# Kernel tuning notes

Measured on AMD Instinct MI355X. Metric: run time of the kernel, lower is better.

## Reference

```python
import jax, jax.numpy as jnp
import numpy as np

H = 128
N_NODES = 100000
N_EDGES = 400000
N_INC = 800000
BN_EPS = 1e-5


def _bn_relu(x, g, b):
    # BatchNorm1d in training mode: batch mean + biased variance, then affine + ReLU
    m = x.mean(0)
    v = x.var(0)
    return jax.nn.relu(g * (x - m) * jax.lax.rsqrt(v + BN_EPS) + b)


def setup_inputs() -> dict:
    key = jax.random.key(0)
    ks = jax.random.split(key, 12)
    s1 = 1.0 / np.sqrt(2 * H)
    s2 = 1.0 / np.sqrt(H)
    inp = {
        "node_rep": jax.random.normal(ks[0], (N_NODES, H), jnp.float32),
        "edge_rep": jax.random.normal(ks[1], (N_EDGES, H), jnp.float32),
        "node_idx": jax.random.randint(ks[2], (N_INC,), 0, N_NODES),
        "edge_idx": jax.random.randint(ks[3], (N_INC,), 0, N_EDGES),
        # lvl_mlp_1: Linear(2H->H, no bias) + BN + ReLU
        "W1": jax.random.uniform(ks[4], (2 * H, H), jnp.float32, -s1, s1),
        "g1": jnp.ones((H,), jnp.float32), "b1": jnp.zeros((H,), jnp.float32),
        # lvl_mlp_2: two (Linear(H->H,no bias)+BN+ReLU) blocks
        "W2a": jax.random.uniform(ks[5], (H, H), jnp.float32, -s2, s2),
        "g2a": jnp.ones((H,), jnp.float32), "b2a": jnp.zeros((H,), jnp.float32),
        "W2b": jax.random.uniform(ks[6], (H, H), jnp.float32, -s2, s2),
        "g2b": jnp.ones((H,), jnp.float32), "b2b": jnp.zeros((H,), jnp.float32),
        # lift_mlp: two (Linear(H->H,no bias)+BN+ReLU) blocks
        "W3a": jax.random.uniform(ks[7], (H, H), jnp.float32, -s2, s2),
        "g3a": jnp.ones((H,), jnp.float32), "b3a": jnp.zeros((H,), jnp.float32),
        "W3b": jax.random.uniform(ks[8], (H, H), jnp.float32, -s2, s2),
        "g3b": jnp.ones((H,), jnp.float32), "b3b": jnp.zeros((H,), jnp.float32),
        "eps1": jnp.zeros((), jnp.float32),
        "eps2": jnp.zeros((), jnp.float32),
    }
    return inp


def reference(node_rep, edge_rep, node_idx, edge_idx,
              W1, g1, b1, W2a, g2a, b2a, W2b, g2b, b2b,
              W3a, g3a, b3a, W3b, g3b, b3b, eps1, eps2):
    n2e_val = node_rep[node_idx]                          # [M,H] gather
    msg = jnp.concatenate([n2e_val, edge_rep[edge_idx]], -1)  # [M,2H]
    msg = _bn_relu(msg @ W1, g1, b1)                      # lvl_mlp_1 -> [M,H]
    cat = jax.ops.segment_sum(jnp.concatenate([msg, n2e_val], -1),
                              edge_idx, num_segments=edge_rep.shape[0])  # [E,2H]
    lvl_aggr_edge = cat[:, :H][edge_idx] - msg            # [M,H]
    lift_aggr = cat[:, H:]                                # [E,H]
    lvl_aggr = jax.ops.segment_sum(lvl_aggr_edge, node_idx,
                                   num_segments=node_rep.shape[0])  # [N,H]
    x = (1.0 + eps1) * node_rep + lvl_aggr
    node_out = _bn_relu(_bn_relu(x @ W2a, g2a, b2a) @ W2b, g2b, b2b)
    y = (1.0 + eps2) * edge_rep + lift_aggr
    edge_out = _bn_relu(_bn_relu(y @ W3a, g3a, b3a) @ W3b, g3b, b3b)
    return node_out, edge_out
```

## Files before the change

kernel.cpp:

```cpp
#include <hip/hip_runtime.h>

#define H 128
#define N_NODES 100000
#define N_EDGES 400000
#define N_INC   800000
#define BN_EPS 1e-5f

typedef __attribute__((ext_vector_type(8))) __bf16 bf16x8;
typedef __attribute__((ext_vector_type(4))) float f32x4;

__device__ __forceinline__ float4 ld4(const float* p) { return *(const float4*)p; }
__device__ __forceinline__ void st4(float* p, float4 v) { *(float4*)p = v; }
__device__ __forceinline__ float4 bnrelu4(float4 p, float4 sc, float4 sf) {
    float4 o;
    o.x = fmaxf(fmaf(p.x, sc.x, sf.x), 0.f);
    o.y = fmaxf(fmaf(p.y, sc.y, sf.y), 0.f);
    o.z = fmaxf(fmaf(p.z, sc.z, sf.z), 0.f);
    o.w = fmaxf(fmaf(p.w, sc.w, sf.w), 0.f);
    return o;
}
__device__ __forceinline__ unsigned short f2bf(float x) {
    unsigned int u = __builtin_bit_cast(unsigned int, x);
    u += 0x7fffu + ((u >> 16) & 1u);
    return (unsigned short)(u >> 16);
}
__device__ __forceinline__ float bf2f(unsigned short s) {
    unsigned int u = ((unsigned int)s) << 16;
    return __builtin_bit_cast(float, u);
}

__device__ __forceinline__ void split8(const float* a, bf16x8& h, bf16x8& l) {
#pragma unroll
    for (int j = 0; j < 8; ++j) h[j] = (__bf16)a[j];
#pragma unroll
    for (int j = 0; j < 8; ++j) l[j] = (__bf16)(a[j] - (float)h[j]);
}

__global__ void wtrans_kernel(const float* __restrict__ W, unsigned short* __restrict__ Wt,
                              int kbits)
{
    int i = blockIdx.x * 256 + threadIdx.x;
    int K = 1 << kbits;
    int n = i >> kbits;
    int k = i & (K - 1);
    Wt[i] = f2bf(W[(size_t)k * H + n]);
}


__global__ __launch_bounds__(256) void gemm1_mfma(
    const float* __restrict__ node_rep, const float* __restrict__ edge_rep,
    const int* __restrict__ node_idx, const int* __restrict__ edge_idx,
    const unsigned short* __restrict__ Wt,
    unsigned short* __restrict__ out, float* __restrict__ sums)
{
    const int tid = threadIdx.x;
    const int lane = tid & 63;
    const int wv = tid >> 6;
    const int l15 = lane & 15;
    const int kb = lane >> 4;
    const int ko = kb * 8;
    const int rowBase = blockIdx.x * 128 + wv * 32;
    const int r0 = rowBase + l15;
    const int r1 = rowBase + 16 + l15;
    const float* an0 = node_rep + (size_t)node_idx[r0] * H;
    const float* ae0 = edge_rep + (size_t)edge_idx[r0] * H;
    const float* an1 = node_rep + (size_t)node_idx[r1] * H;
    const float* ae1 = edge_rep + (size_t)edge_idx[r1] * H;

    f32x4 acc[2][8];
#pragma unroll
    for (int i = 0; i < 2; ++i)
#pragma unroll
        for (int j = 0; j < 8; ++j) acc[i][j] = (f32x4){0.f, 0.f, 0.f, 0.f};

#pragma unroll
    for (int ks = 0; ks < 8; ++ks) {
        const int k0 = ks * 32 + ko;
        const float* p0 = (ks < 4) ? (an0 + k0) : (ae0 + (k0 - 128));
        const float* p1 = (ks < 4) ? (an1 + k0) : (ae1 + (k0 - 128));
        float a0[8], a1[8];
        { float4 x = ld4(p0), y = ld4(p0 + 4);
          a0[0]=x.x; a0[1]=x.y; a0[2]=x.z; a0[3]=x.w; a0[4]=y.x; a0[5]=y.y; a0[6]=y.z; a0[7]=y.w; }
        { float4 x = ld4(p1), y = ld4(p1 + 4);
          a1[0]=x.x; a1[1]=x.y; a1[2]=x.z; a1[3]=x.w; a1[4]=y.x; a1[5]=y.y; a1[6]=y.z; a1[7]=y.w; }
        bf16x8 h0, l0, h1, l1;
        split8(a0, h0, l0);
        split8(a1, h1, l1);
        const unsigned short* wp = Wt + (size_t)l15 * 256 + ks * 32 + ko;
#pragma unroll
        for (int ct = 0; ct < 8; ++ct) {
            bf16x8 bw = *(const bf16x8*)(wp + ct * 16 * 256);
            acc[0][ct] = __builtin_amdgcn_mfma_f32_16x16x32_bf16(h0, bw, acc[0][ct], 0, 0, 0);
            acc[0][ct] = __builtin_amdgcn_mfma_f32_16x16x32_bf16(l0, bw, acc[0][ct], 0, 0, 0);
            acc[1][ct] = __builtin_amdgcn_mfma_f32_16x16x32_bf16(h1, bw, acc[1][ct], 0, 0, 0);
            acc[1][ct] = __builtin_amdgcn_mfma_f32_16x16x32_bf16(l1, bw, acc[1][ct], 0, 0, 0);
        }
    }

    __shared__ float sred[4][256];
    float scol[8], qcol[8];
#pragma unroll
    for (int ct = 0; ct < 8; ++ct) { scol[ct] = 0.f; qcol[ct] = 0.f; }
#pragma unroll
    for (int rt = 0; rt < 2; ++rt) {
        const int rg = rowBase + rt * 16 + kb * 4;
#pragma unroll
        for (int j = 0; j < 4; ++j) {
#pragma unroll
            for (int ct = 0; ct < 8; ++ct) {
                unsigned short us = f2bf(acc[rt][ct][j]);
                out[(size_t)(rg + j) * H + ct * 16 + l15] = us;
                float v = bf2f(us);
                scol[ct] += v;
                qcol[ct] = fmaf(v, v, qcol[ct]);
            }
        }
    }
#pragma unroll
    for (int ct = 0; ct < 8; ++ct) {
        scol[ct] += __shfl_xor(scol[ct], 16);
        scol[ct] += __shfl_xor(scol[ct], 32);
        qcol[ct] += __shfl_xor(qcol[ct], 16);
        qcol[ct] += __shfl_xor(qcol[ct], 32);
    }
    if (kb == 0) {
#pragma unroll
        for (int ct = 0; ct < 8; ++ct) {
            sred[wv][ct * 16 + l15] = scol[ct];
            sred[wv][128 + ct * 16 + l15] = qcol[ct];
        }
    }
    __syncthreads();
    float tot = sred[0][tid & 255] + sred[1][tid & 255] + sred[2][tid & 255] + sred[3][tid & 255];
    atomicAdd(&sums[tid & 255], tot);
}

__global__ __launch_bounds__(256) void gemmh_mfma(
    int M, int mode, const float* __restrict__ A0, const float* __restrict__ ss,
    const unsigned short* __restrict__ Wt,
    float* __restrict__ out, float* __restrict__ sums)
{
    const int tid = threadIdx.x;
    const int lane = tid & 63;
    const int wv = tid >> 6;
    const int l15 = lane & 15;
    const int kb = lane >> 4;
    const int ko = kb * 8;
    const int rowBase = blockIdx.x * 128 + wv * 32;
    int r0 = rowBase + l15;       if (r0 >= M) r0 = M - 1;
    int r1 = rowBase + 16 + l15;  if (r1 >= M) r1 = M - 1;
    const float* a0p = A0 + (size_t)r0 * H;
    const float* a1p = A0 + (size_t)r1 * H;

    f32x4 acc[2][8];
#pragma unroll
    for (int i = 0; i < 2; ++i)
#pragma unroll
        for (int j = 0; j < 8; ++j) acc[i][j] = (f32x4){0.f, 0.f, 0.f, 0.f};

#pragma unroll
    for (int ks = 0; ks < 4; ++ks) {
        const int k0 = ks * 32 + ko;
        float a0[8], a1[8];
        { float4 x = ld4(a0p + k0), y = ld4(a0p + k0 + 4);
          a0[0]=x.x; a0[1]=x.y; a0[2]=x.z; a0[3]=x.w; a0[4]=y.x; a0[5]=y.y; a0[6]=y.z; a0[7]=y.w; }
        { float4 x = ld4(a1p + k0), y = ld4(a1p + k0 + 4);
          a1[0]=x.x; a1[1]=x.y; a1[2]=x.z; a1[3]=x.w; a1[4]=y.x; a1[5]=y.y; a1[6]=y.z; a1[7]=y.w; }
        if (mode == 2) {
            float4 sca = ld4(&ss[k0]), scb = ld4(&ss[k0 + 4]);
            float4 sfa = ld4(&ss[128 + k0]), sfb = ld4(&ss[128 + k0 + 4]);
            float sc[8] = {sca.x, sca.y, sca.z, sca.w, scb.x, scb.y, scb.z, scb.w};
            float sf[8] = {sfa.x, sfa.y, sfa.z, sfa.w, sfb.x, sfb.y, sfb.z, sfb.w};
#pragma unroll
            for (int j = 0; j < 8; ++j) {
                a0[j] = fmaxf(fmaf(a0[j], sc[j], sf[j]), 0.f);
                a1[j] = fmaxf(fmaf(a1[j], sc[j], sf[j]), 0.f);
            }
        }
        bf16x8 h0, l0, h1, l1;
        split8(a0, h0, l0);
        split8(a1, h1, l1);
        const unsigned short* wp = Wt + (size_t)l15 * 128 + ks * 32 + ko;
#pragma unroll
        for (int ct = 0; ct < 8; ++ct) {
            bf16x8 bw = *(const bf16x8*)(wp + ct * 16 * 128);
            acc[0][ct] = __builtin_amdgcn_mfma_f32_16x16x32_bf16(h0, bw, acc[0][ct], 0, 0, 0);
            acc[0][ct] = __builtin_amdgcn_mfma_f32_16x16x32_bf16(l0, bw, acc[0][ct], 0, 0, 0);
            acc[1][ct] = __builtin_amdgcn_mfma_f32_16x16x32_bf16(h1, bw, acc[1][ct], 0, 0, 0);
            acc[1][ct] = __builtin_amdgcn_mfma_f32_16x16x32_bf16(l1, bw, acc[1][ct], 0, 0, 0);
        }
    }

    __shared__ float sred[4][256];
    float scol[8], qcol[8];
#pragma unroll
    for (int ct = 0; ct < 8; ++ct) { scol[ct] = 0.f; qcol[ct] = 0.f; }
#pragma unroll
    for (int rt = 0; rt < 2; ++rt) {
#pragma unroll
        for (int j = 0; j < 4; ++j) {
            const int rg = rowBase + rt * 16 + kb * 4 + j;
            if (rg < M) {
#pragma unroll
                for (int ct = 0; ct < 8; ++ct) {
                    float v = acc[rt][ct][j];
                    out[(size_t)rg * H + ct * 16 + l15] = v;
                    scol[ct] += v;
                    qcol[ct] = fmaf(v, v, qcol[ct]);
                }
            }
        }
    }
#pragma unroll
    for (int ct = 0; ct < 8; ++ct) {
        scol[ct] += __shfl_xor(scol[ct], 16);
        scol[ct] += __shfl_xor(scol[ct], 32);
        qcol[ct] += __shfl_xor(qcol[ct], 16);
        qcol[ct] += __shfl_xor(qcol[ct], 32);
    }
    if (kb == 0) {
#pragma unroll
        for (int ct = 0; ct < 8; ++ct) {
            sred[wv][ct * 16 + l15] = scol[ct];
            sred[wv][128 + ct * 16 + l15] = qcol[ct];
        }
    }
    __syncthreads();
    float tot = sred[0][tid & 255] + sred[1][tid & 255] + sred[2][tid & 255] + sred[3][tid & 255];
    atomicAdd(&sums[tid & 255], tot);
}

__global__ void finalize_kernel(const float* __restrict__ sums, float invM,
                                const float* __restrict__ g, const float* __restrict__ b,
                                float* __restrict__ ss)
{
    int c = threadIdx.x;
    float mean = sums[c] * invM;
    float var = fmaf(-mean, mean, sums[128 + c] * invM);
    float scale = g[c] * rsqrtf(var + BN_EPS);
    ss[c] = scale;
    ss[128 + c] = fmaf(-mean, scale, b[c]);
}

__global__ void hist_kernel(const int* __restrict__ idx, int* __restrict__ cnt, int n)
{
    int i = blockIdx.x * 256 + threadIdx.x;
    if (i < n) atomicAdd(&cnt[idx[i]], 1);
}

__global__ __launch_bounds__(256) void scan_block_kernel(int* __restrict__ a, int n,
                                                         int* __restrict__ aux)
{
    __shared__ int sh[2048];
    __shared__ int ts[256];
    const int t = threadIdx.x;
    const int base = blockIdx.x * 2048;
#pragma unroll
    for (int k = 0; k < 8; ++k) {
        int i = base + t + k * 256;
        sh[t + k * 256] = (i < n) ? a[i] : 0;
    }
    __syncthreads();
    int loc[8], sum = 0;
#pragma unroll
    for (int k = 0; k < 8; ++k) { loc[k] = sh[t * 8 + k]; sum += loc[k]; }
    ts[t] = sum;
    __syncthreads();
    for (int o = 1; o < 256; o <<= 1) {
        int v = (t >= o) ? ts[t - o] : 0;
        __syncthreads();
        ts[t] += v;
        __syncthreads();
    }
    int run = ts[t] - sum;
#pragma unroll
    for (int k = 0; k < 8; ++k) {
        int i = base + t * 8 + k;
        if (i < n) a[i] = run;
        run += loc[k];
    }
    if (aux != nullptr && t == 255) aux[blockIdx.x] = ts[255];
}

__global__ void scan_add_kernel(int* __restrict__ a, int n, const int* __restrict__ aux)
{
    int i = blockIdx.x * 256 + threadIdx.x;
    if (i < n) a[i] += aux[i >> 11];
}

__global__ void fill_kernel(const int* __restrict__ idx, int* __restrict__ off,
                            int* __restrict__ list, int n)
{
    int i = blockIdx.x * 256 + threadIdx.x;
    if (i < n) {
        int p = atomicAdd(&off[idx[i]], 1);
        list[p] = i;
    }
}

__global__ __launch_bounds__(256) void gather_edge_kernel(
    const unsigned short* __restrict__ msg, const float* __restrict__ node_rep,
    const float* __restrict__ edge_rep, const int* __restrict__ node_idx,
    const int* __restrict__ eoff, const int* __restrict__ elist,
    const float* __restrict__ ss, const float* __restrict__ eps2p,
    float* __restrict__ catm, float* __restrict__ yedge)
{
    const int t = threadIdx.x;
    const int sub = t >> 5;
    const int lane = t & 31;
    const int e = blockIdx.x * 8 + sub;
    const int c = lane * 4;
    const int s = (e == 0) ? 0 : eoff[e - 1];
    const int en = eoff[e];
    const float4 sc = ld4(&ss[c]);
    const float4 sf = ld4(&ss[128 + c]);
    float4 macc = make_float4(0.f, 0.f, 0.f, 0.f);
    float4 lacc = make_float4(0.f, 0.f, 0.f, 0.f);
    int idx = (s < en) ? elist[s] : 0;
    for (int j = s; j < en; ++j) {
        int idxn = (j + 1 < en) ? elist[j + 1] : 0;
        int n = node_idx[idx];
        ushort4 mb = *(const ushort4*)(msg + (size_t)idx * H + c);
        float4 nv = ld4(&node_rep[(size_t)n * H + c]);
        float4 p = make_float4(bf2f(mb.x), bf2f(mb.y), bf2f(mb.z), bf2f(mb.w));
        float4 m = bnrelu4(p, sc, sf);
        macc.x += m.x; macc.y += m.y; macc.z += m.z; macc.w += m.w;
        lacc.x += nv.x; lacc.y += nv.y; lacc.z += nv.z; lacc.w += nv.w;
        idx = idxn;
    }
    st4(&catm[(size_t)e * H + c], macc);
    const float eps = eps2p[0];
    float4 er = ld4(&edge_rep[(size_t)e * H + c]);
    float4 y;
    y.x = fmaf(eps, er.x, er.x + lacc.x);
    y.y = fmaf(eps, er.y, er.y + lacc.y);
    y.z = fmaf(eps, er.z, er.z + lacc.z);
    y.w = fmaf(eps, er.w, er.w + lacc.w);
    st4(&yedge[(size_t)e * H + c], y);
}

__global__ __launch_bounds__(256) void gather_node_kernel(
    const unsigned short* __restrict__ msg, const float* __restrict__ catm,
    const float* __restrict__ node_rep, const int* __restrict__ edge_idx,
    const int* __restrict__ noff, const int* __restrict__ nlist,
    const float* __restrict__ ss, const float* __restrict__ eps1p,
    float* __restrict__ xnode)
{
    const int t = threadIdx.x;
    const int sub = t >> 5;
    const int lane = t & 31;
    const int n = blockIdx.x * 8 + sub;
    const int c = lane * 4;
    const int s = (n == 0) ? 0 : noff[n - 1];
    const int en = noff[n];
    const float4 sc = ld4(&ss[c]);
    const float4 sf = ld4(&ss[128 + c]);
    float4 acc = make_float4(0.f, 0.f, 0.f, 0.f);
    int idx = (s < en) ? nlist[s] : 0;
    for (int j = s; j < en; ++j) {
        int idxn = (j + 1 < en) ? nlist[j + 1] : 0;
        int e = edge_idx[idx];
        ushort4 mb = *(const ushort4*)(msg + (size_t)idx * H + c);
        float4 cv = ld4(&catm[(size_t)e * H + c]);
        float4 p = make_float4(bf2f(mb.x), bf2f(mb.y), bf2f(mb.z), bf2f(mb.w));
        float4 m = bnrelu4(p, sc, sf);
        acc.x += cv.x - m.x; acc.y += cv.y - m.y;
        acc.z += cv.z - m.z; acc.w += cv.w - m.w;
        idx = idxn;
    }
    const float eps = eps1p[0];
    float4 nr = ld4(&node_rep[(size_t)n * H + c]);
    float4 x;
    x.x = fmaf(eps, nr.x, nr.x + acc.x);
    x.y = fmaf(eps, nr.y, nr.y + acc.y);
    x.z = fmaf(eps, nr.z, nr.z + acc.z);
    x.w = fmaf(eps, nr.w, nr.w + acc.w);
    st4(&xnode[(size_t)n * H + c], x);
}

__global__ __launch_bounds__(256) void apply_kernel(const float* __restrict__ pre,
                                                    const float* __restrict__ ss,
                                                    float* __restrict__ out, int M)
{
    size_t gid = (size_t)blockIdx.x * 256 + threadIdx.x;
    size_t r = gid >> 5;
    int c = (int)(gid & 31) * 4;
    if (r >= (size_t)M) return;
    float4 p = ld4(&pre[r * H + c]);
    float4 sc = ld4(&ss[c]);
    float4 sf = ld4(&ss[128 + c]);
    st4(&out[r * H + c], bnrelu4(p, sc, sf));
}

extern "C" void kernel_launch(void* const* d_in, const int* in_sizes, int n_in,
                              void* d_out, int out_size, void* d_ws, size_t ws_size,
                              hipStream_t stream)
{
    const float* node_rep = (const float*)d_in[0];
    const float* edge_rep = (const float*)d_in[1];
    const int*   node_idx = (const int*)d_in[2];
    const int*   edge_idx = (const int*)d_in[3];
    const float* W1  = (const float*)d_in[4];
    const float* g1  = (const float*)d_in[5];
    const float* b1  = (const float*)d_in[6];
    const float* W2a = (const float*)d_in[7];
    const float* g2a = (const float*)d_in[8];
    const float* b2a = (const float*)d_in[9];
    const float* W2b = (const float*)d_in[10];
    const float* g2b = (const float*)d_in[11];
    const float* b2b = (const float*)d_in[12];
    const float* W3a = (const float*)d_in[13];
    const float* g3a = (const float*)d_in[14];
    const float* b3a = (const float*)d_in[15];
    const float* W3b = (const float*)d_in[16];
    const float* g3b = (const float*)d_in[17];
    const float* b3b = (const float*)d_in[18];
    const float* eps1 = (const float*)d_in[19];
    const float* eps2 = (const float*)d_in[20];

    float* ws = (float*)d_ws;
    unsigned short* msgb = (unsigned short*)ws;
    float* catm  = ws + (size_t) 51200000;
    float* yedge = ws + (size_t)102400000;
    float* xnode = ws + (size_t)153600000;
    int* eoff  = (int*)(ws + (size_t)153600000);
    int* elist = (int*)(ws + (size_t)154000000);
    float* stat = ws + (size_t)166400000;
    int* noff  = (int*)(ws + (size_t)166402560);
    int* nlist = (int*)(ws + (size_t)166502560);
    int* eaux  = (int*)(ws + (size_t)167302560);
    int* naux  = (int*)(ws + (size_t)167302816);
    unsigned short* wt1  = (unsigned short*)(ws + (size_t)167304000);
    unsigned short* wt2a = (unsigned short*)(ws + (size_t)167320384);
    unsigned short* wt2b = (unsigned short*)(ws + (size_t)167328576);
    unsigned short* wt3a = (unsigned short*)(ws + (size_t)167336768);
    unsigned short* wt3b = (unsigned short*)(ws + (size_t)167344960);

    float* e1 = catm;
    float* e2 = (float*)msgb;
    float* n1 = catm;
    float* n2 = catm + (size_t)12800000;

    float* sums0 = stat +    0; float* ss0 = stat + 1280;
    float* sums1 = stat +  256; float* ss1 = stat + 1536;
    float* sums2 = stat +  512; float* ss2 = stat + 1792;
    float* sums3 = stat +  768; float* ss3 = stat + 2048;
    float* sums4 = stat + 1024; float* ss4 = stat + 2304;

    float* out_node = (float*)d_out;
    float* out_edge = out_node + (size_t)N_NODES * H;

    hipMemsetAsync(stat, 0, 1280 * sizeof(float), stream);
    hipMemsetAsync(eoff, 0, (size_t)N_EDGES * sizeof(int), stream);
    hipMemsetAsync(noff, 0, (size_t)N_NODES * sizeof(int), stream);

    wtrans_kernel<<<128, 256, 0, stream>>>(W1,  wt1,  8);
    wtrans_kernel<<< 64, 256, 0, stream>>>(W2a, wt2a, 7);
    wtrans_kernel<<< 64, 256, 0, stream>>>(W2b, wt2b, 7);
    wtrans_kernel<<< 64, 256, 0, stream>>>(W3a, wt3a, 7);
    wtrans_kernel<<< 64, 256, 0, stream>>>(W3b, wt3b, 7);

    hist_kernel<<<N_INC / 256, 256, 0, stream>>>(edge_idx, eoff, N_INC);
    scan_block_kernel<<<196, 256, 0, stream>>>(eoff, N_EDGES, eaux);
    scan_block_kernel<<<1, 256, 0, stream>>>(eaux, 196, nullptr);
    scan_add_kernel<<<(N_EDGES + 255) / 256, 256, 0, stream>>>(eoff, N_EDGES, eaux);
    fill_kernel<<<N_INC / 256, 256, 0, stream>>>(edge_idx, eoff, elist, N_INC);

    hist_kernel<<<N_INC / 256, 256, 0, stream>>>(node_idx, noff, N_INC);
    scan_block_kernel<<<49, 256, 0, stream>>>(noff, N_NODES, naux);
    scan_block_kernel<<<1, 256, 0, stream>>>(naux, 49, nullptr);
    scan_add_kernel<<<(N_NODES + 255) / 256, 256, 0, stream>>>(noff, N_NODES, naux);
    fill_kernel<<<N_INC / 256, 256, 0, stream>>>(node_idx, noff, nlist, N_INC);

    gemm1_mfma<<<N_INC / 128, 256, 0, stream>>>(node_rep, edge_rep, node_idx, edge_idx,
                                                wt1, msgb, sums0);
    finalize_kernel<<<1, 128, 0, stream>>>(sums0, 1.0f / N_INC, g1, b1, ss0);

    gather_edge_kernel<<<N_EDGES / 8, 256, 0, stream>>>(msgb, node_rep, edge_rep, node_idx,
                                                        eoff, elist, ss0, eps2, catm, yedge);
    gather_node_kernel<<<N_NODES / 8, 256, 0, stream>>>(msgb, catm, node_rep, edge_idx,
                                                        noff, nlist, ss0, eps1, xnode);

    gemmh_mfma<<<N_EDGES / 128, 256, 0, stream>>>(N_EDGES, 0, yedge, nullptr, wt3a, e1, sums3);
    finalize_kernel<<<1, 128, 0, stream>>>(sums3, 1.0f / N_EDGES, g3a, b3a, ss3);
    gemmh_mfma<<<N_EDGES / 128, 256, 0, stream>>>(N_EDGES, 2, e1, ss3, wt3b, e2, sums4);
    finalize_kernel<<<1, 128, 0, stream>>>(sums4, 1.0f / N_EDGES, g3b, b3b, ss4);
    apply_kernel<<<N_EDGES / 8, 256, 0, stream>>>(e2, ss4, out_edge, N_EDGES);

    gemmh_mfma<<<(N_NODES + 127) / 128, 256, 0, stream>>>(N_NODES, 0, xnode, nullptr, wt2a, n1, sums1);
    finalize_kernel<<<1, 128, 0, stream>>>(sums1, 1.0f / N_NODES, g2a, b2a, ss1);
    gemmh_mfma<<<(N_NODES + 127) / 128, 256, 0, stream>>>(N_NODES, 2, n1, ss1, wt2b, n2, sums2);
    finalize_kernel<<<1, 128, 0, stream>>>(sums2, 1.0f / N_NODES, g2b, b2b, ss2);
    apply_kernel<<<N_NODES / 8, 256, 0, stream>>>(n2, ss2, out_node, N_NODES);
}
```

Baseline: 1.822 ms.

## Stage weights in swizzled LDS, use persistent blocks, and prefetch A tiles

Each GEMM kernel now copies its transposed bf16 weight matrix into LDS once per block, with an XOR swizzle against bank conflicts. The grid becomes persistent: a fixed number of blocks loop over row tiles and keep BN column statistics in registers, so there are fewer atomics and less weight reloading. A three-slot register buffer prefetches A rows two k-steps ahead to hide gather latency. The cost is a large LDS footprint (64KB for gemm1) that limits occupancy, plus more registers per thread.

Result: faster. 1.715 ms (-5.9%).

```diff
diff --git a/kernel.cpp b/kernel.cpp
--- a/kernel.cpp
+++ b/kernel.cpp
@@ -53,69 +53,94 @@
     const unsigned short* __restrict__ Wt,
     unsigned short* __restrict__ out, float* __restrict__ sums)
 {
+    __shared__ unsigned short Wl[128 * 256];
     const int tid = threadIdx.x;
     const int lane = tid & 63;
     const int wv = tid >> 6;
     const int l15 = lane & 15;
     const int kb = lane >> 4;
     const int ko = kb * 8;
-    const int rowBase = blockIdx.x * 128 + wv * 32;
-    const int r0 = rowBase + l15;
-    const int r1 = rowBase + 16 + l15;
-    const float* an0 = node_rep + (size_t)node_idx[r0] * H;
-    const float* ae0 = edge_rep + (size_t)edge_idx[r0] * H;
-    const float* an1 = node_rep + (size_t)node_idx[r1] * H;
-    const float* ae1 = edge_rep + (size_t)edge_idx[r1] * H;
-
-    f32x4 acc[2][8];
-#pragma unroll
-    for (int i = 0; i < 2; ++i)
-#pragma unroll
-        for (int j = 0; j < 8; ++j) acc[i][j] = (f32x4){0.f, 0.f, 0.f, 0.f};
-
-#pragma unroll
-    for (int ks = 0; ks < 8; ++ks) {
-        const int k0 = ks * 32 + ko;
-        const float* p0 = (ks < 4) ? (an0 + k0) : (ae0 + (k0 - 128));
-        const float* p1 = (ks < 4) ? (an1 + k0) : (ae1 + (k0 - 128));
-        float a0[8], a1[8];
-        { float4 x = ld4(p0), y = ld4(p0 + 4);
-          a0[0]=x.x; a0[1]=x.y; a0[2]=x.z; a0[3]=x.w; a0[4]=y.x; a0[5]=y.y; a0[6]=y.z; a0[7]=y.w; }
-        { float4 x = ld4(p1), y = ld4(p1 + 4);
-          a1[0]=x.x; a1[1]=x.y; a1[2]=x.z; a1[3]=x.w; a1[4]=y.x; a1[5]=y.y; a1[6]=y.z; a1[7]=y.w; }
-        bf16x8 h0, l0, h1, l1;
-        split8(a0, h0, l0);
-        split8(a1, h1, l1);
-        const unsigned short* wp = Wt + (size_t)l15 * 256 + ks * 32 + ko;
-#pragma unroll
-        for (int ct = 0; ct < 8; ++ct) {
-            bf16x8 bw = *(const bf16x8*)(wp + ct * 16 * 256);
-            acc[0][ct] = __builtin_amdgcn_mfma_f32_16x16x32_bf16(h0, bw, acc[0][ct], 0, 0, 0);
-            acc[0][ct] = __builtin_amdgcn_mfma_f32_16x16x32_bf16(l0, bw, acc[0][ct], 0, 0, 0);
-            acc[1][ct] = __builtin_amdgcn_mfma_f32_16x16x32_bf16(h1, bw, acc[1][ct], 0, 0, 0);
-            acc[1][ct] = __builtin_amdgcn_mfma_f32_16x16x32_bf16(l1, bw, acc[1][ct], 0, 0, 0);
+    const int swz = (l15 & 7) << 3;
+
+#pragma unroll
+    for (int it = 0; it < 16; ++it) {
+        int g = it * 256 + tid;
+        int n = g >> 5, k8 = (g & 31) * 8;
+        *(uint4*)&Wl[n * 256 + (k8 ^ ((n & 7) << 3))] = *(const uint4*)&Wt[(size_t)n * 256 + k8];
+    }
+    __syncthreads();
+
+    float scol[8], qcol[8];
+#pragma unroll
+    for (int ct = 0; ct < 8; ++ct) { scol[ct] = 0.f; qcol[ct] = 0.f; }
+
+    for (int rb = blockIdx.x; rb < N_INC / 128; rb += gridDim.x) {
+        const int rowBase = rb * 128 + wv * 32;
+        const int r0 = rowBase + l15;
+        const int r1 = rowBase + 16 + l15;
+        const float* an0 = node_rep + (size_t)node_idx[r0] * H + ko;
+        const float* ae0 = edge_rep + (size_t)edge_idx[r0] * H + ko;
+        const float* an1 = node_rep + (size_t)node_idx[r1] * H + ko;
+        const float* ae1 = edge_rep + (size_t)edge_idx[r1] * H + ko;
+
+        f32x4 acc[2][8];
+#pragma unroll
+        for (int i = 0; i < 2; ++i)
+#pragma unroll
+            for (int j = 0; j < 8; ++j) acc[i][j] = (f32x4){0.f, 0.f, 0.f, 0.f};
+
+        float4 ab[3][2][2];
+        ab[0][0][0] = ld4(an0);      ab[0][0][1] = ld4(an0 + 4);
+        ab[0][1][0] = ld4(an1);      ab[0][1][1] = ld4(an1 + 4);
+        ab[1][0][0] = ld4(an0 + 32); ab[1][0][1] = ld4(an0 + 36);
+        ab[1][1][0] = ld4(an1 + 32); ab[1][1][1] = ld4(an1 + 36);
+
+#pragma unroll
+        for (int ks = 0; ks < 8; ++ks) {
+            if (ks < 6) {
+                const int kf = (ks + 2) * 32;
+                const float* p0 = (ks + 2 < 4) ? an0 + kf : ae0 + (kf - 128);
+                const float* p1 = (ks + 2 < 4) ? an1 + kf : ae1 + (kf - 128);
+                const int slot = (ks + 2) % 3;
+                ab[slot][0][0] = ld4(p0); ab[slot][0][1] = ld4(p0 + 4);
+                ab[slot][1][0] = ld4(p1); ab[slot][1][1] = ld4(p1 + 4);
+            }
+            const int cur = ks % 3;
+            float a0[8] = {ab[cur][0][0].x, ab[cur][0][0].y, ab[cur][0][0].z, ab[cur][0][0].w,
+                           ab[cur][0][1].x, ab[cur][0][1].y, ab[cur][0][1].z, ab[cur][0][1].w};
+            float a1[8] = {ab[cur][1][0].x, ab[cur][1][0].y, ab[cur][1][0].z, ab[cur][1][0].w,
+                           ab[cur][1][1].x, ab[cur][1][1].y, ab[cur][1][1].z, ab[cur][1][1].w};
+            bf16x8 h0, l0, h1, l1;
+            split8(a0, h0, l0);
+            split8(a1, h1, l1);
+            const int kbase = (ks * 32 + ko) ^ swz;
+#pragma unroll
+            for (int ct = 0; ct < 8; ++ct) {
+                bf16x8 bw = *(const bf16x8*)&Wl[(ct * 16 + l15) * 256 + kbase];
+                acc[0][ct] = __builtin_amdgcn_mfma_f32_16x16x32_bf16(h0, bw, acc[0][ct], 0, 0, 0);
+                acc[0][ct] = __builtin_amdgcn_mfma_f32_16x16x32_bf16(l0, bw, acc[0][ct], 0, 0, 0);
+                acc[1][ct] = __builtin_amdgcn_mfma_f32_16x16x32_bf16(h1, bw, acc[1][ct], 0, 0, 0);
+                acc[1][ct] = __builtin_amdgcn_mfma_f32_16x16x32_bf16(l1, bw, acc[1][ct], 0, 0, 0);
+            }
         }
-    }
-
-    __shared__ float sred[4][256];
-    float scol[8], qcol[8];
-#pragma unroll
-    for (int ct = 0; ct < 8; ++ct) { scol[ct] = 0.f; qcol[ct] = 0.f; }
-#pragma unroll
-    for (int rt = 0; rt < 2; ++rt) {
-        const int rg = rowBase + rt * 16 + kb * 4;
-#pragma unroll
-        for (int j = 0; j < 4; ++j) {
-#pragma unroll
-            for (int ct = 0; ct < 8; ++ct) {
-                unsigned short us = f2bf(acc[rt][ct][j]);
-                out[(size_t)(rg + j) * H + ct * 16 + l15] = us;
-                float v = bf2f(us);
-                scol[ct] += v;
-                qcol[ct] = fmaf(v, v, qcol[ct]);
+
+#pragma unroll
+        for (int rt = 0; rt < 2; ++rt) {
+            const int rg0 = rowBase + rt * 16 + kb * 4;
+#pragma unroll
+            for (int j = 0; j < 4; ++j) {
+#pragma unroll
+                for (int ct = 0; ct < 8; ++ct) {
+                    unsigned short us = f2bf(acc[rt][ct][j]);
+                    out[(size_t)(rg0 + j) * H + ct * 16 + l15] = us;
+                    float v = bf2f(us);
+                    scol[ct] += v;
+                    qcol[ct] = fmaf(v, v, qcol[ct]);
+                }
             }
         }
     }
+
 #pragma unroll
     for (int ct = 0; ct < 8; ++ct) {
         scol[ct] += __shfl_xor(scol[ct], 16);
@@ -123,94 +148,123 @@
         qcol[ct] += __shfl_xor(qcol[ct], 16);
         qcol[ct] += __shfl_xor(qcol[ct], 32);
     }
+    __syncthreads();
+    float* sred = (float*)Wl;
     if (kb == 0) {
 #pragma unroll
         for (int ct = 0; ct < 8; ++ct) {
-            sred[wv][ct * 16 + l15] = scol[ct];
-            sred[wv][128 + ct * 16 + l15] = qcol[ct];
+            sred[wv * 256 + ct * 16 + l15] = scol[ct];
+            sred[wv * 256 + 128 + ct * 16 + l15] = qcol[ct];
         }
     }
     __syncthreads();
-    float tot = sred[0][tid & 255] + sred[1][tid & 255] + sred[2][tid & 255] + sred[3][tid & 255];
-    atomicAdd(&sums[tid & 255], tot);
-}
-
-__global__ __launch_bounds__(256) void gemmh_mfma(
+    float tot = sred[tid] + sred[256 + tid] + sred[512 + tid] + sred[768 + tid];
+    atomicAdd(&sums[tid], tot);
+}
+
+__global__ __launch_bounds__(256, 3) void gemmh_mfma(
     int M, int mode, const float* __restrict__ A0, const float* __restrict__ ss,
     const unsigned short* __restrict__ Wt,
     float* __restrict__ out, float* __restrict__ sums)
 {
+    __shared__ unsigned short Wl[128 * 128];
     const int tid = threadIdx.x;
     const int lane = tid & 63;
     const int wv = tid >> 6;
     const int l15 = lane & 15;
     const int kb = lane >> 4;
     const int ko = kb * 8;
-    const int rowBase = blockIdx.x * 128 + wv * 32;
-    int r0 = rowBase + l15;       if (r0 >= M) r0 = M - 1;
-    int r1 = rowBase + 16 + l15;  if (r1 >= M) r1 = M - 1;
-    const float* a0p = A0 + (size_t)r0 * H;
-    const float* a1p = A0 + (size_t)r1 * H;
-
-    f32x4 acc[2][8];
-#pragma unroll
-    for (int i = 0; i < 2; ++i)
-#pragma unroll
-        for (int j = 0; j < 8; ++j) acc[i][j] = (f32x4){0.f, 0.f, 0.f, 0.f};
-
-#pragma unroll
-    for (int ks = 0; ks < 4; ++ks) {
-        const int k0 = ks * 32 + ko;
-        float a0[8], a1[8];
-        { float4 x = ld4(a0p + k0), y = ld4(a0p + k0 + 4);
-          a0[0]=x.x; a0[1]=x.y; a0[2]=x.z; a0[3]=x.w; a0[4]=y.x; a0[5]=y.y; a0[6]=y.z; a0[7]=y.w; }
-        { float4 x = ld4(a1p + k0), y = ld4(a1p + k0 + 4);
-          a1[0]=x.x; a1[1]=x.y; a1[2]=x.z; a1[3]=x.w; a1[4]=y.x; a1[5]=y.y; a1[6]=y.z; a1[7]=y.w; }
-        if (mode == 2) {
-            float4 sca = ld4(&ss[k0]), scb = ld4(&ss[k0 + 4]);
-            float4 sfa = ld4(&ss[128 + k0]), sfb = ld4(&ss[128 + k0 + 4]);
-            float sc[8] = {sca.x, sca.y, sca.z, sca.w, scb.x, scb.y, scb.z, scb.w};
-            float sf[8] = {sfa.x, sfa.y, sfa.z, sfa.w, sfb.x, sfb.y, sfb.z, sfb.w};
-#pragma unroll
-            for (int j = 0; j < 8; ++j) {
-                a0[j] = fmaxf(fmaf(a0[j], sc[j], sf[j]), 0.f);
-                a1[j] = fmaxf(fmaf(a1[j], sc[j], sf[j]), 0.f);
+    const int swz = (l15 & 7) << 3;
+    const int nTiles = (M + 127) >> 7;
+
+#pragma unroll
+    for (int it = 0; it < 8; ++it) {
+        int g = it * 256 + tid;
+        int n = g >> 4, k8 = (g & 15) * 8;
+        *(uint4*)&Wl[n * 128 + (k8 ^ ((n & 7) << 3))] = *(const uint4*)&Wt[(size_t)n * 128 + k8];
+    }
+    __syncthreads();
+
+    float scol[8], qcol[8];
+#pragma unroll
+    for (int ct = 0; ct < 8; ++ct) { scol[ct] = 0.f; qcol[ct] = 0.f; }
+
+    for (int rb = blockIdx.x; rb < nTiles; rb += gridDim.x) {
+        const int rowBase = rb * 128 + wv * 32;
+        int r0 = rowBase + l15;       if (r0 >= M) r0 = M - 1;
+        int r1 = rowBase + 16 + l15;  if (r1 >= M) r1 = M - 1;
+        const float* a0p = A0 + (size_t)r0 * H + ko;
+        const float* a1p = A0 + (size_t)r1 * H + ko;
+
+        f32x4 acc[2][8];
+#pragma unroll
+        for (int i = 0; i < 2; ++i)
+#pragma unroll
+            for (int j = 0; j < 8; ++j) acc[i][j] = (f32x4){0.f, 0.f, 0.f, 0.f};
+
+        float4 ab[3][2][2];
+        ab[0][0][0] = ld4(a0p);      ab[0][0][1] = ld4(a0p + 4);
+        ab[0][1][0] = ld4(a1p);      ab[0][1][1] = ld4(a1p + 4);
+        ab[1][0][0] = ld4(a0p + 32); ab[1][0][1] = ld4(a0p + 36);
+        ab[1][1][0] = ld4(a1p + 32); ab[1][1][1] = ld4(a1p + 36);
+
+#pragma unroll
+        for (int ks = 0; ks < 4; ++ks) {
+            if (ks < 2) {
+                const int kf = (ks + 2) * 32;
+                const int slot = (ks + 2) % 3;
+                ab[slot][0][0] = ld4(a0p + kf); ab[slot][0][1] = ld4(a0p + kf + 4);
+                ab[slot][1][0] = ld4(a1p + kf); ab[slot][1][1] = ld4(a1p + kf + 4);
+            }
+            const int cur = ks % 3;
+            float a0[8] = {ab[cur][0][0].x, ab[cur][0][0].y, ab[cur][0][0].z, ab[cur][0][0].w,
+                           ab[cur][0][1].x, ab[cur][0][1].y, ab[cur][0][1].z, ab[cur][0][1].w};
+            float a1[8] = {ab[cur][1][0].x, ab[cur][1][0].y, ab[cur][1][0].z, ab[cur][1][0].w,
+                           ab[cur][1][1].x, ab[cur][1][1].y, ab[cur][1][1].z, ab[cur][1][1].w};
+            if (mode == 2) {
+                const int k0 = ks * 32 + ko;
+                float4 sca = ld4(&ss[k0]), scb = ld4(&ss[k0 + 4]);
+                float4 sfa = ld4(&ss[128 + k0]), sfb = ld4(&ss[128 + k0 + 4]);
+                float sc[8] = {sca.x, sca.y, sca.z, sca.w, scb.x, scb.y, scb.z, scb.w};
+                float sf[8] = {sfa.x, sfa.y, sfa.z, sfa.w, sfb.x, sfb.y, sfb.z, sfb.w};
+#pragma unroll
+                for (int j = 0; j < 8; ++j) {
+                    a0[j] = fmaxf(fmaf(a0[j], sc[j], sf[j]), 0.f);
+                    a1[j] = fmaxf(fmaf(a1[j], sc[j], sf[j]), 0.f);
+                }
+            }
+            bf16x8 h0, l0, h1, l1;
+            split8(a0, h0, l0);
+            split8(a1, h1, l1);
+            const int kbase = (ks * 32 + ko) ^ swz;
+#pragma unroll
+            for (int ct = 0; ct < 8; ++ct) {
+                bf16x8 bw = *(const bf16x8*)&Wl[(ct * 16 + l15) * 128 + kbase];
+                acc[0][ct] = __builtin_amdgcn_mfma_f32_16x16x32_bf16(h0, bw, acc[0][ct], 0, 0, 0);
+                acc[0][ct] = __builtin_amdgcn_mfma_f32_16x16x32_bf16(l0, bw, acc[0][ct], 0, 0, 0);
+                acc[1][ct] = __builtin_amdgcn_mfma_f32_16x16x32_bf16(h1, bw, acc[1][ct], 0, 0, 0);
+                acc[1][ct] = __builtin_amdgcn_mfma_f32_16x16x32_bf16(l1, bw, acc[1][ct], 0, 0, 0);
             }
         }
-        bf16x8 h0, l0, h1, l1;
-        split8(a0, h0, l0);
-        split8(a1, h1, l1);
-        const unsigned short* wp = Wt + (size_t)l15 * 128 + ks * 32 + ko;
-#pragma unroll
-        for (int ct = 0; ct < 8; ++ct) {
-            bf16x8 bw = *(const bf16x8*)(wp + ct * 16 * 128);
-            acc[0][ct] = __builtin_amdgcn_mfma_f32_16x16x32_bf16(h0, bw, acc[0][ct], 0, 0, 0);
-            acc[0][ct] = __builtin_amdgcn_mfma_f32_16x16x32_bf16(l0, bw, acc[0][ct], 0, 0, 0);
-            acc[1][ct] = __builtin_amdgcn_mfma_f32_16x16x32_bf16(h1, bw, acc[1][ct], 0, 0, 0);
-            acc[1][ct] = __builtin_amdgcn_mfma_f32_16x16x32_bf16(l1, bw, acc[1][ct], 0, 0, 0);
+
+#pragma unroll
+        for (int rt = 0; rt < 2; ++rt) {
+#pragma unroll
+            for (int j = 0; j < 4; ++j) {
+                const int rg = rowBase + rt * 16 + kb * 4 + j;
+                if (rg < M) {
+#pragma unroll
+                    for (int ct = 0; ct < 8; ++ct) {
+                        float v = acc[rt][ct][j];
+                        out[(size_t)rg * H + ct * 16 + l15] = v;
+                        scol[ct] += v;
+                        qcol[ct] = fmaf(v, v, qcol[ct]);
+                    }
+                }
+            }
         }
     }
 
-    __shared__ float sred[4][256];
-    float scol[8], qcol[8];
-#pragma unroll
-    for (int ct = 0; ct < 8; ++ct) { scol[ct] = 0.f; qcol[ct] = 0.f; }
-#pragma unroll
-    for (int rt = 0; rt < 2; ++rt) {
-#pragma unroll
-        for (int j = 0; j < 4; ++j) {
-            const int rg = rowBase + rt * 16 + kb * 4 + j;
-            if (rg < M) {
-#pragma unroll
-                for (int ct = 0; ct < 8; ++ct) {
-                    float v = acc[rt][ct][j];
-                    out[(size_t)rg * H + ct * 16 + l15] = v;
-                    scol[ct] += v;
-                    qcol[ct] = fmaf(v, v, qcol[ct]);
-                }
-            }
-        }
-    }
 #pragma unroll
     for (int ct = 0; ct < 8; ++ct) {
         scol[ct] += __shfl_xor(scol[ct], 16);
@@ -218,16 +272,18 @@
         qcol[ct] += __shfl_xor(qcol[ct], 16);
         qcol[ct] += __shfl_xor(qcol[ct], 32);
     }
+    __syncthreads();
+    float* sred = (float*)Wl;
     if (kb == 0) {
 #pragma unroll
         for (int ct = 0; ct < 8; ++ct) {
-            sred[wv][ct * 16 + l15] = scol[ct];
-            sred[wv][128 + ct * 16 + l15] = qcol[ct];
+            sred[wv * 256 + ct * 16 + l15] = scol[ct];
+            sred[wv * 256 + 128 + ct * 16 + l15] = qcol[ct];
         }
     }
     __syncthreads();
-    float tot = sred[0][tid & 255] + sred[1][tid & 255] + sred[2][tid & 255] + sred[3][tid & 255];
-    atomicAdd(&sums[tid & 255], tot);
+    float tot = sred[tid] + sred[256 + tid] + sred[512 + tid] + sred[768 + tid];
+    atomicAdd(&sums[tid], tot);
 }
 
 __global__ void finalize_kernel(const float* __restrict__ sums, float invM,
@@ -472,8 +528,8 @@
     scan_add_kernel<<<(N_NODES + 255) / 256, 256, 0, stream>>>(noff, N_NODES, naux);
     fill_kernel<<<N_INC / 256, 256, 0, stream>>>(node_idx, noff, nlist, N_INC);
 
-    gemm1_mfma<<<N_INC / 128, 256, 0, stream>>>(node_rep, edge_rep, node_idx, edge_idx,
-                                                wt1, msgb, sums0);
+    gemm1_mfma<<<512, 256, 0, stream>>>(node_rep, edge_rep, node_idx, edge_idx,
+                                        wt1, msgb, sums0);
     finalize_kernel<<<1, 128, 0, stream>>>(sums0, 1.0f / N_INC, g1, b1, ss0);
 
     gather_edge_kernel<<<N_EDGES / 8, 256, 0, stream>>>(msgb, node_rep, edge_rep, node_idx,
@@ -481,15 +537,15 @@
     gather_node_kernel<<<N_NODES / 8, 256, 0, stream>>>(msgb, catm, node_rep, edge_idx,
                                                         noff, nlist, ss0, eps1, xnode);
 
-    gemmh_mfma<<<N_EDGES / 128, 256, 0, stream>>>(N_EDGES, 0, yedge, nullptr, wt3a, e1, sums3);
+    gemmh_mfma<<<768, 256, 0, stream>>>(N_EDGES, 0, yedge, nullptr, wt3a, e1, sums3);
     finalize_kernel<<<1, 128, 0, stream>>>(sums3, 1.0f / N_EDGES, g3a, b3a, ss3);
-    gemmh_mfma<<<N_EDGES / 128, 256, 0, stream>>>(N_EDGES, 2, e1, ss3, wt3b, e2, sums4);
+    gemmh_mfma<<<768, 256, 0, stream>>>(N_EDGES, 2, e1, ss3, wt3b, e2, sums4);
     finalize_kernel<<<1, 128, 0, stream>>>(sums4, 1.0f / N_EDGES, g3b, b3b, ss4);
     apply_kernel<<<N_EDGES / 8, 256, 0, stream>>>(e2, ss4, out_edge, N_EDGES);
 
-    gemmh_mfma<<<(N_NODES + 127) / 128, 256, 0, stream>>>(N_NODES, 0, xnode, nullptr, wt2a, n1, sums1);
+    gemmh_mfma<<<768, 256, 0, stream>>>(N_NODES, 0, xnode, nullptr, wt2a, n1, sums1);
     finalize_kernel<<<1, 128, 0, stream>>>(sums1, 1.0f / N_NODES, g2a, b2a, ss1);
-    gemmh_mfma<<<(N_NODES + 127) / 128, 256, 0, stream>>>(N_NODES, 2, n1, ss1, wt2b, n2, sums2);
+    gemmh_mfma<<<768, 256, 0, stream>>>(N_NODES, 2, n1, ss1, wt2b, n2, sums2);
     finalize_kernel<<<1, 128, 0, stream>>>(sums2, 1.0f / N_NODES, g2b, b2b, ss2);
     apply_kernel<<<N_NODES / 8, 256, 0, stream>>>(n2, ss2, out_node, N_NODES);
 }
```
